# Kernel tuning notes

Measured on AMD Instinct MI355X. Metric: run time of the kernel, lower is better.

Reference implementation:

```python
import jax, jax.numpy as jnp
import numpy as np

N = 10000
E = 320000
D_IN = 512
D_OUT = 256


def setup_inputs() -> dict:
    key = jax.random.key(0)
    ks = jax.random.split(key, 10)
    x = jax.random.normal(ks[0], (N, D_IN), dtype=jnp.float32)
    edge_index = jax.random.randint(ks[1], (2, E), 0, N, dtype=jnp.int64)
    s_in = 1.0 / np.sqrt(D_IN)
    s_out = 1.0 / np.sqrt(D_OUT)
    W0 = jax.random.uniform(ks[2], (D_IN, D_OUT), minval=-s_in, maxval=s_in, dtype=jnp.float32)
    b0 = jax.random.uniform(ks[3], (D_OUT,), minval=-s_in, maxval=s_in, dtype=jnp.float32)
    Wl1 = jax.random.uniform(ks[4], (D_OUT, D_OUT), minval=-s_out, maxval=s_out, dtype=jnp.float32)
    bl1 = jax.random.uniform(ks[5], (D_OUT,), minval=-s_out, maxval=s_out, dtype=jnp.float32)
    Wr1 = jax.random.uniform(ks[6], (D_OUT, D_OUT), minval=-s_out, maxval=s_out, dtype=jnp.float32)
    Wl2 = jax.random.uniform(ks[7], (D_OUT, D_OUT), minval=-s_out, maxval=s_out, dtype=jnp.float32)
    bl2 = jax.random.uniform(ks[8], (D_OUT,), minval=-s_out, maxval=s_out, dtype=jnp.float32)
    Wr2 = jax.random.uniform(ks[9], (D_OUT, D_OUT), minval=-s_out, maxval=s_out, dtype=jnp.float32)
    return {"x": x, "edge_index": edge_index, "W0": W0, "b0": b0,
            "Wl1": Wl1, "bl1": bl1, "Wr1": Wr1,
            "Wl2": Wl2, "bl2": bl2, "Wr2": Wr2}


def _sage_conv(h, src, dst, Wl, bl, Wr):
    # mean aggregation over incoming edges: msg j->i uses h[src], summed at dst
    msg = h[src]                                        # [E, D]
    agg = jax.ops.segment_sum(msg, dst, num_segments=N)  # [N, D]
    deg = jax.ops.segment_sum(jnp.ones((msg.shape[0],), h.dtype), dst, num_segments=N)
    mean = agg / jnp.maximum(deg, 1.0)[:, None]
    return mean @ Wl + bl + h @ Wr


def reference(x, edge_index, W0, b0, Wl1, bl1, Wr1, Wl2, bl2, Wr2):
    src, dst = edge_index[0], edge_index[1]
    h = x @ W0 + b0                 # lin; dropout = identity (eval mode)
    out1 = jax.nn.relu(_sage_conv(h, src, dst, Wl1, bl1, Wr1)) + h
    out2 = _sage_conv(out1, src, dst, Wl2, bl2, Wr2) + out1
    return (out1, out2)
```

## Files before the change

kernel.cpp:

```cpp
#include <hip/hip_runtime.h>
#include <cstdint>

#define N_NODES 10000
#define N_EDGES 320000
#define DIN 512
#define DOUT 256
#define DEG_CAP 96

using short8 = __attribute__((ext_vector_type(8))) short;
using f32x4  = __attribute__((ext_vector_type(4))) float;
typedef unsigned short ushort_t;

static __device__ __forceinline__ unsigned short f2bf(float f) {
  unsigned u = __builtin_bit_cast(unsigned, f);
  u += 0x7fffu + ((u >> 16) & 1u);
  return (unsigned short)(u >> 16);
}
static __device__ __forceinline__ float bf2f(unsigned short s) {
  unsigned u = ((unsigned)s) << 16;
  return __builtin_bit_cast(float, u);
}

static __device__ __forceinline__ int detect64(const unsigned* ei) {
  unsigned z = 0;
  #pragma unroll
  for (int i = 1; i < 32; i += 2) z |= ei[i];
  return z == 0u;
}
static __device__ __forceinline__ int load_idx(const unsigned* ei, int i, int is64) {
  return is64 ? (int)ei[2 * i] : (int)ei[i];
}

#define B_EDGE 1250
#define B_W    1536
#define B_X    5000
__global__ __launch_bounds__(256) void prep_all(
    const unsigned* __restrict__ ei, int* __restrict__ cnt,
    int* __restrict__ srcs,
    const float* __restrict__ x, ushort_t* __restrict__ xb,
    const float* __restrict__ W0,
    const float* __restrict__ Wl1, const float* __restrict__ Wr1,
    const float* __restrict__ Wl2, const float* __restrict__ Wr2,
    ushort_t* __restrict__ W0T, ushort_t* __restrict__ WT1,
    ushort_t* __restrict__ WT2) {
  int b = blockIdx.x;
  if (b < B_EDGE) {
    int is64 = detect64(ei);
    int e = b * 256 + threadIdx.x;
    int d = load_idx(ei, N_EDGES + e, is64);
    int s = load_idx(ei, e, is64);
    int pos = atomicAdd(&cnt[d], 1);
    if (pos < DEG_CAP) srcs[d * DEG_CAP + pos] = s;
  } else if (b < B_EDGE + B_W) {
    int g = (b - B_EDGE) * 256 + threadIdx.x;
    int mat = g >> 17;
    int r = g & 131071;
    int n = r >> 9, k = r & 511;
    float v;
    ushort_t* dst;
    if (mat == 0)      { v = W0[k * 256 + n]; dst = W0T; }
    else if (mat == 1) { v = (k < 256) ? Wl1[k * 256 + n] : Wr1[(k - 256) * 256 + n]; dst = WT1; }
    else               { v = (k < 256) ? Wl2[k * 256 + n] : Wr2[(k - 256) * 256 + n]; dst = WT2; }
    dst[r] = f2bf(v);
  } else {
    int g = (b - B_EDGE - B_W) * 256 + threadIdx.x;
    float4 f = *(const float4*)(x + (size_t)g * 4);
    uint2 o;
    o.x = (unsigned)f2bf(f.x) | ((unsigned)f2bf(f.y) << 16);
    o.y = (unsigned)f2bf(f.z) | ((unsigned)f2bf(f.w) << 16);
    *(uint2*)(xb + (size_t)g * 4) = o;
  }
}

__global__ __launch_bounds__(256) void agg_mean(const ushort_t* __restrict__ h,
                                                const int* __restrict__ cnt,
                                                const int* __restrict__ srcs,
                                                ushort_t* __restrict__ mean) {
  int node = blockIdx.x * 4 + (threadIdx.x >> 6);
  int lane = threadIdx.x & 63;
  if (node >= N_NODES) return;
  int deg = cnt[node];
  int d = (deg < DEG_CAP) ? deg : DEG_CAP;
  int beg = node * DEG_CAP;
  int end = beg + d;
  float a0 = 0.f, a1 = 0.f, a2 = 0.f, a3 = 0.f;
  int j = beg;
  for (; j + 16 <= end; j += 16) {
    int4 sa = *(const int4*)(srcs + j);
    int4 sb = *(const int4*)(srcs + j + 4);
    int4 sc = *(const int4*)(srcs + j + 8);
    int4 sd = *(const int4*)(srcs + j + 12);
    uint2 u0 = *(const uint2*)(h + (size_t)sa.x * 256 + lane * 4);
    uint2 u1 = *(const uint2*)(h + (size_t)sa.y * 256 + lane * 4);
    uint2 u2 = *(const uint2*)(h + (size_t)sa.z * 256 + lane * 4);
    uint2 u3 = *(const uint2*)(h + (size_t)sa.w * 256 + lane * 4);
    uint2 u4 = *(const uint2*)(h + (size_t)sb.x * 256 + lane * 4);
    uint2 u5 = *(const uint2*)(h + (size_t)sb.y * 256 + lane * 4);
    uint2 u6 = *(const uint2*)(h + (size_t)sb.z * 256 + lane * 4);
    uint2 u7 = *(const uint2*)(h + (size_t)sb.w * 256 + lane * 4);
    uint2 u8 = *(const uint2*)(h + (size_t)sc.x * 256 + lane * 4);
    uint2 u9 = *(const uint2*)(h + (size_t)sc.y * 256 + lane * 4);
    uint2 ua = *(const uint2*)(h + (size_t)sc.z * 256 + lane * 4);
    uint2 ub = *(const uint2*)(h + (size_t)sc.w * 256 + lane * 4);
    uint2 uc = *(const uint2*)(h + (size_t)sd.x * 256 + lane * 4);
    uint2 ud = *(const uint2*)(h + (size_t)sd.y * 256 + lane * 4);
    uint2 ue = *(const uint2*)(h + (size_t)sd.z * 256 + lane * 4);
    uint2 uf = *(const uint2*)(h + (size_t)sd.w * 256 + lane * 4);
    a0 += bf2f(u0.x & 0xffff) + bf2f(u1.x & 0xffff) + bf2f(u2.x & 0xffff) + bf2f(u3.x & 0xffff);
    a1 += bf2f(u0.x >> 16)    + bf2f(u1.x >> 16)    + bf2f(u2.x >> 16)    + bf2f(u3.x >> 16);
    a2 += bf2f(u0.y & 0xffff) + bf2f(u1.y & 0xffff) + bf2f(u2.y & 0xffff) + bf2f(u3.y & 0xffff);
    a3 += bf2f(u0.y >> 16)    + bf2f(u1.y >> 16)    + bf2f(u2.y >> 16)    + bf2f(u3.y >> 16);
    a0 += bf2f(u4.x & 0xffff) + bf2f(u5.x & 0xffff) + bf2f(u6.x & 0xffff) + bf2f(u7.x & 0xffff);
    a1 += bf2f(u4.x >> 16)    + bf2f(u5.x >> 16)    + bf2f(u6.x >> 16)    + bf2f(u7.x >> 16);
    a2 += bf2f(u4.y & 0xffff) + bf2f(u5.y & 0xffff) + bf2f(u6.y & 0xffff) + bf2f(u7.y & 0xffff);
    a3 += bf2f(u4.y >> 16)    + bf2f(u5.y >> 16)    + bf2f(u6.y >> 16)    + bf2f(u7.y >> 16);
    a0 += bf2f(u8.x & 0xffff) + bf2f(u9.x & 0xffff) + bf2f(ua.x & 0xffff) + bf2f(ub.x & 0xffff);
    a1 += bf2f(u8.x >> 16)    + bf2f(u9.x >> 16)    + bf2f(ua.x >> 16)    + bf2f(ub.x >> 16);
    a2 += bf2f(u8.y & 0xffff) + bf2f(u9.y & 0xffff) + bf2f(ua.y & 0xffff) + bf2f(ub.y & 0xffff);
    a3 += bf2f(u8.y >> 16)    + bf2f(u9.y >> 16)    + bf2f(ua.y >> 16)    + bf2f(ub.y >> 16);
    a0 += bf2f(uc.x & 0xffff) + bf2f(ud.x & 0xffff) + bf2f(ue.x & 0xffff) + bf2f(uf.x & 0xffff);
    a1 += bf2f(uc.x >> 16)    + bf2f(ud.x >> 16)    + bf2f(ue.x >> 16)    + bf2f(uf.x >> 16);
    a2 += bf2f(uc.y & 0xffff) + bf2f(ud.y & 0xffff) + bf2f(ue.y & 0xffff) + bf2f(uf.y & 0xffff);
    a3 += bf2f(uc.y >> 16)    + bf2f(ud.y >> 16)    + bf2f(ue.y >> 16)    + bf2f(uf.y >> 16);
  }
  for (; j + 8 <= end; j += 8) {
    int4 sa = *(const int4*)(srcs + j);
    int4 sb = *(const int4*)(srcs + j + 4);
    uint2 u0 = *(const uint2*)(h + (size_t)sa.x * 256 + lane * 4);
    uint2 u1 = *(const uint2*)(h + (size_t)sa.y * 256 + lane * 4);
    uint2 u2 = *(const uint2*)(h + (size_t)sa.z * 256 + lane * 4);
    uint2 u3 = *(const uint2*)(h + (size_t)sa.w * 256 + lane * 4);
    uint2 u4 = *(const uint2*)(h + (size_t)sb.x * 256 + lane * 4);
    uint2 u5 = *(const uint2*)(h + (size_t)sb.y * 256 + lane * 4);
    uint2 u6 = *(const uint2*)(h + (size_t)sb.z * 256 + lane * 4);
    uint2 u7 = *(const uint2*)(h + (size_t)sb.w * 256 + lane * 4);
    a0 += bf2f(u0.x & 0xffff) + bf2f(u1.x & 0xffff) + bf2f(u2.x & 0xffff) + bf2f(u3.x & 0xffff);
    a1 += bf2f(u0.x >> 16)    + bf2f(u1.x >> 16)    + bf2f(u2.x >> 16)    + bf2f(u3.x >> 16);
    a2 += bf2f(u0.y & 0xffff) + bf2f(u1.y & 0xffff) + bf2f(u2.y & 0xffff) + bf2f(u3.y & 0xffff);
    a3 += bf2f(u0.y >> 16)    + bf2f(u1.y >> 16)    + bf2f(u2.y >> 16)    + bf2f(u3.y >> 16);
    a0 += bf2f(u4.x & 0xffff) + bf2f(u5.x & 0xffff) + bf2f(u6.x & 0xffff) + bf2f(u7.x & 0xffff);
    a1 += bf2f(u4.x >> 16)    + bf2f(u5.x >> 16)    + bf2f(u6.x >> 16)    + bf2f(u7.x >> 16);
    a2 += bf2f(u4.y & 0xffff) + bf2f(u5.y & 0xffff) + bf2f(u6.y & 0xffff) + bf2f(u7.y & 0xffff);
    a3 += bf2f(u4.y >> 16)    + bf2f(u5.y >> 16)    + bf2f(u6.y >> 16)    + bf2f(u7.y >> 16);
  }
  for (; j + 4 <= end; j += 4) {
    int4 s4 = *(const int4*)(srcs + j);
    uint2 u0 = *(const uint2*)(h + (size_t)s4.x * 256 + lane * 4);
    uint2 u1 = *(const uint2*)(h + (size_t)s4.y * 256 + lane * 4);
    uint2 u2 = *(const uint2*)(h + (size_t)s4.z * 256 + lane * 4);
    uint2 u3 = *(const uint2*)(h + (size_t)s4.w * 256 + lane * 4);
    a0 += bf2f(u0.x & 0xffff) + bf2f(u1.x & 0xffff) + bf2f(u2.x & 0xffff) + bf2f(u3.x & 0xffff);
    a1 += bf2f(u0.x >> 16)    + bf2f(u1.x >> 16)    + bf2f(u2.x >> 16)    + bf2f(u3.x >> 16);
    a2 += bf2f(u0.y & 0xffff) + bf2f(u1.y & 0xffff) + bf2f(u2.y & 0xffff) + bf2f(u3.y & 0xffff);
    a3 += bf2f(u0.y >> 16)    + bf2f(u1.y >> 16)    + bf2f(u2.y >> 16)    + bf2f(u3.y >> 16);
  }
  for (; j < end; ++j) {
    int s0 = srcs[j];
    uint2 u0 = *(const uint2*)(h + (size_t)s0 * 256 + lane * 4);
    a0 += bf2f(u0.x & 0xffff);
    a1 += bf2f(u0.x >> 16);
    a2 += bf2f(u0.y & 0xffff);
    a3 += bf2f(u0.y >> 16);
  }
  float inv = 1.0f / (float)(d > 1 ? d : 1);
  a0 *= inv; a1 *= inv; a2 *= inv; a3 *= inv;
  uint2 o;
  o.x = (unsigned)f2bf(a0) | ((unsigned)f2bf(a1) << 16);
  o.y = (unsigned)f2bf(a2) | ((unsigned)f2bf(a3) << 16);
  *(uint2*)(mean + (size_t)node * 256 + lane * 4) = o;
}

template<int DO_RELU, int HAS_ADD, int HAS_OUTF, int HAS_OUTB, int SPLIT_A>
__global__ __launch_bounds__(256) void gemm_pan(
    const ushort_t* __restrict__ A0, const ushort_t* __restrict__ A1,
    const ushort_t* __restrict__ BT, const float* __restrict__ bias,
    const ushort_t* __restrict__ addB,
    float* __restrict__ outF, ushort_t* __restrict__ outB, int M) {
  __shared__ ushort_t Bs[64 * 520];

  const int bid = blockIdx.x;
  const int sg  = bid >> 5;
  const int r32 = bid & 31;
  const int xt  = (sg << 3) + (r32 & 7);
  const int yt  = r32 >> 3;
  const int xtiles = (M + 127) >> 7;
  if (xt >= xtiles) return;

  const int tid  = threadIdx.x;
  const int lane = tid & 63;
  const int w    = tid >> 6;
  const int bn   = yt * 64;
  const int mbase = xt * 128 + w * 32;

  #pragma unroll
  for (int i = 0; i < 16; ++i) {
    int c = i * 256 + tid;
    int row = c >> 6;
    int c8  = (c & 63) * 8;
    uint4 bv = *(const uint4*)(BT + (size_t)(bn + row) * 512 + c8);
    *(uint4*)&Bs[row * 520 + c8] = bv;
  }
  __syncthreads();

  f32x4 acc[2][4] = {};
  const int mrow = lane & 15;
  const int k8   = (lane >> 4) * 8;

  #pragma unroll
  for (int kt = 0; kt < 512; kt += 32) {
    const ushort_t* Asrc;
    int acol, ald;
    if (SPLIT_A) {
      if (kt < 256) { Asrc = A0; acol = kt; } else { Asrc = A1; acol = kt - 256; }
      ald = 256;
    } else {
      Asrc = A0; acol = kt; ald = 512;
    }
    short8 a[2], b[4];
    #pragma unroll
    for (int s = 0; s < 2; ++s) {
      int row = mbase + s * 16 + mrow;
      a[s] = *(const short8*)(Asrc + (size_t)row * ald + acol + k8);
    }
    #pragma unroll
    for (int ni = 0; ni < 4; ++ni)
      b[ni] = *(const short8*)&Bs[(ni * 16 + mrow) * 520 + kt + k8];
    #pragma unroll
    for (int s = 0; s < 2; ++s)
      #pragma unroll
      for (int ni = 0; ni < 4; ++ni)
        acc[s][ni] = __builtin_amdgcn_mfma_f32_16x16x32_bf16(a[s], b[ni], acc[s][ni], 0, 0, 0);
  }

  const int cq   = lane >> 4;
  const int ccol = lane & 15;
  #pragma unroll
  for (int ni = 0; ni < 4; ++ni) {
    int gcol = bn + ni * 16 + ccol;
    float bv = bias[gcol];
    #pragma unroll
    for (int s = 0; s < 2; ++s) {
      #pragma unroll
      for (int r = 0; r < 4; ++r) {
        int grow = mbase + s * 16 + cq * 4 + r;
        if (grow < M) {
          float v = acc[s][ni][r] + bv;
          if (DO_RELU) v = fmaxf(v, 0.f);
          if (HAS_ADD) v += bf2f(addB[(size_t)grow * DOUT + gcol]);
          if (HAS_OUTF) __builtin_nontemporal_store(v, &outF[(size_t)grow * DOUT + gcol]);
          if (HAS_OUTB) outB[(size_t)grow * DOUT + gcol] = f2bf(v);
        }
      }
    }
  }
}

extern "C" void kernel_launch(void* const* d_in, const int* in_sizes, int n_in,
                              void* d_out, int out_size, void* d_ws, size_t ws_size,
                              hipStream_t stream) {
  const float*    x   = (const float*)d_in[0];
  const unsigned* ei  = (const unsigned*)d_in[1];
  const float*    W0  = (const float*)d_in[2];
  const float*    b0  = (const float*)d_in[3];
  const float*    Wl1 = (const float*)d_in[4];
  const float*    bl1 = (const float*)d_in[5];
  const float*    Wr1 = (const float*)d_in[6];
  const float*    Wl2 = (const float*)d_in[7];
  const float*    bl2 = (const float*)d_in[8];
  const float*    Wr2 = (const float*)d_in[9];

  char* ws = (char*)d_ws;
  size_t off = 0;
  auto alloc = [&](size_t bytes) {
    char* p = ws + off;
    off += (bytes + 255) & ~(size_t)255;
    return p;
  };
  ushort_t* xb  = (ushort_t*)alloc((size_t)N_NODES * 512 * 2);
  ushort_t* hb  = (ushort_t*)alloc((size_t)N_NODES * 256 * 2);
  ushort_t* o1b = (ushort_t*)alloc((size_t)N_NODES * 256 * 2);
  ushort_t* mb  = (ushort_t*)alloc((size_t)N_NODES * 256 * 2);
  ushort_t* W0T = (ushort_t*)alloc(256 * 512 * 2);
  ushort_t* WT1 = (ushort_t*)alloc(256 * 512 * 2);
  ushort_t* WT2 = (ushort_t*)alloc(256 * 512 * 2);
  int* cnt    = (int*)alloc(N_NODES * 4);
  int* srcs   = (int*)alloc((size_t)N_NODES * DEG_CAP * 4);

  float* out1 = (float*)d_out;
  float* out2 = out1 + (size_t)N_NODES * DOUT;

  hipMemsetAsync(cnt, 0, N_NODES * 4, stream);
  prep_all<<<B_EDGE + B_W + B_X, 256, 0, stream>>>(ei, cnt, srcs, x, xb,
                                                   W0, Wl1, Wr1, Wl2, Wr2,
                                                   W0T, WT1, WT2);

  const int GG = 320;
  gemm_pan<0, 0, 0, 1, 0><<<GG, 256, 0, stream>>>(xb, nullptr, W0T, b0, nullptr,
                                                  nullptr, hb, N_NODES);
  agg_mean<<<(N_NODES + 3) / 4, 256, 0, stream>>>(hb, cnt, srcs, mb);
  gemm_pan<1, 1, 1, 1, 1><<<GG, 256, 0, stream>>>(mb, hb, WT1, bl1, hb,
                                                  out1, o1b, N_NODES);
  agg_mean<<<(N_NODES + 3) / 4, 256, 0, stream>>>(o1b, cnt, srcs, mb);
  gemm_pan<0, 1, 1, 0, 1><<<GG, 256, 0, stream>>>(mb, o1b, WT2, bl2, o1b,
                                                  out2, nullptr, N_NODES);
}
```

Before: 196.0 us.

## Fuse root-weight GEMM into aggregation kernel and pre-pack weights in MFMA fragment layout

```diff
diff --git a/kernel.cpp b/kernel.cpp
--- a/kernel.cpp
+++ b/kernel.cpp
@@ -6,6 +6,7 @@
 #define DIN 512
 #define DOUT 256
 #define DEG_CAP 96
+#define AGGB 2500
 
 using short8 = __attribute__((ext_vector_type(8))) short;
 using f32x4  = __attribute__((ext_vector_type(4))) float;
@@ -41,8 +42,9 @@
     const float* __restrict__ W0,
     const float* __restrict__ Wl1, const float* __restrict__ Wr1,
     const float* __restrict__ Wl2, const float* __restrict__ Wr2,
-    ushort_t* __restrict__ W0T, ushort_t* __restrict__ WT1,
-    ushort_t* __restrict__ WT2) {
+    ushort_t* __restrict__ W0P,
+    ushort_t* __restrict__ WlP1, ushort_t* __restrict__ WrP1,
+    ushort_t* __restrict__ WlP2, ushort_t* __restrict__ WrP2) {
   int b = blockIdx.x;
   if (b < B_EDGE) {
     int is64 = detect64(ei);
@@ -55,13 +57,22 @@
     int g = (b - B_EDGE) * 256 + threadIdx.x;
     int mat = g >> 17;
     int r = g & 131071;
-    int n = r >> 9, k = r & 511;
-    float v;
-    ushort_t* dst;
-    if (mat == 0)      { v = W0[k * 256 + n]; dst = W0T; }
-    else if (mat == 1) { v = (k < 256) ? Wl1[k * 256 + n] : Wr1[(k - 256) * 256 + n]; dst = WT1; }
-    else               { v = (k < 256) ? Wl2[k * 256 + n] : Wr2[(k - 256) * 256 + n]; dst = WT2; }
-    dst[r] = f2bf(v);
+    if (mat == 0) {
+      int tile = r >> 9, e2 = r & 511;
+      int l = e2 >> 3, j = e2 & 7, q = l >> 4, rr = l & 15;
+      int nb = tile >> 4, kb = tile & 15;
+      int n = nb * 16 + rr, k = kb * 32 + q * 8 + j;
+      W0P[r] = f2bf(W0[k * 256 + n]);
+    } else {
+      int half = r >> 16, rr2 = r & 65535;
+      int tile = rr2 >> 9, e2 = rr2 & 511;
+      int l = e2 >> 3, j = e2 & 7, q = l >> 4, rr = l & 15;
+      int nb = tile >> 3, kb = tile & 7;
+      int n = nb * 16 + rr, k = kb * 32 + q * 8 + j;
+      const float* W = (mat == 1) ? (half ? Wr1 : Wl1) : (half ? Wr2 : Wl2);
+      ushort_t* P    = (mat == 1) ? (half ? WrP1 : WlP1) : (half ? WrP2 : WlP2);
+      P[rr2] = f2bf(W[k * 256 + n]);
+    }
   } else {
     int g = (b - B_EDGE - B_W) * 256 + threadIdx.x;
     float4 f = *(const float4*)(x + (size_t)g * 4);
@@ -72,13 +83,11 @@
   }
 }
 
-__global__ __launch_bounds__(256) void agg_mean(const ushort_t* __restrict__ h,
-                                                const int* __restrict__ cnt,
-                                                const int* __restrict__ srcs,
-                                                ushort_t* __restrict__ mean) {
-  int node = blockIdx.x * 4 + (threadIdx.x >> 6);
+static __device__ __forceinline__ void agg_body(
+    int grp, const ushort_t* __restrict__ h, const int* __restrict__ cnt,
+    const int* __restrict__ srcs, ushort_t* __restrict__ mean) {
+  int node = grp * 4 + (threadIdx.x >> 6);
   int lane = threadIdx.x & 63;
-  if (node >= N_NODES) return;
   int deg = cnt[node];
   int d = (deg < DEG_CAP) ? deg : DEG_CAP;
   int beg = node * DEG_CAP;
@@ -123,26 +132,6 @@
     a2 += bf2f(uc.y & 0xffff) + bf2f(ud.y & 0xffff) + bf2f(ue.y & 0xffff) + bf2f(uf.y & 0xffff);
     a3 += bf2f(uc.y >> 16)    + bf2f(ud.y >> 16)    + bf2f(ue.y >> 16)    + bf2f(uf.y >> 16);
   }
-  for (; j + 8 <= end; j += 8) {
-    int4 sa = *(const int4*)(srcs + j);
-    int4 sb = *(const int4*)(srcs + j + 4);
-    uint2 u0 = *(const uint2*)(h + (size_t)sa.x * 256 + lane * 4);
-    uint2 u1 = *(const uint2*)(h + (size_t)sa.y * 256 + lane * 4);
-    uint2 u2 = *(const uint2*)(h + (size_t)sa.z * 256 + lane * 4);
-    uint2 u3 = *(const uint2*)(h + (size_t)sa.w * 256 + lane * 4);
-    uint2 u4 = *(const uint2*)(h + (size_t)sb.x * 256 + lane * 4);
-    uint2 u5 = *(const uint2*)(h + (size_t)sb.y * 256 + lane * 4);
-    uint2 u6 = *(const uint2*)(h + (size_t)sb.z * 256 + lane * 4);
-    uint2 u7 = *(const uint2*)(h + (size_t)sb.w * 256 + lane * 4);
-    a0 += bf2f(u0.x & 0xffff) + bf2f(u1.x & 0xffff) + bf2f(u2.x & 0xffff) + bf2f(u3.x & 0xffff);
-    a1 += bf2f(u0.x >> 16)    + bf2f(u1.x >> 16)    + bf2f(u2.x >> 16)    + bf2f(u3.x >> 16);
-    a2 += bf2f(u0.y & 0xffff) + bf2f(u1.y & 0xffff) + bf2f(u2.y & 0xffff) + bf2f(u3.y & 0xffff);
-    a3 += bf2f(u0.y >> 16)    + bf2f(u1.y >> 16)    + bf2f(u2.y >> 16)    + bf2f(u3.y >> 16);
-    a0 += bf2f(u4.x & 0xffff) + bf2f(u5.x & 0xffff) + bf2f(u6.x & 0xffff) + bf2f(u7.x & 0xffff);
-    a1 += bf2f(u4.x >> 16)    + bf2f(u5.x >> 16)    + bf2f(u6.x >> 16)    + bf2f(u7.x >> 16);
-    a2 += bf2f(u4.y & 0xffff) + bf2f(u5.y & 0xffff) + bf2f(u6.y & 0xffff) + bf2f(u7.y & 0xffff);
-    a3 += bf2f(u4.y >> 16)    + bf2f(u5.y >> 16)    + bf2f(u6.y >> 16)    + bf2f(u7.y >> 16);
-  }
   for (; j + 4 <= end; j += 4) {
     int4 s4 = *(const int4*)(srcs + j);
     uint2 u0 = *(const uint2*)(h + (size_t)s4.x * 256 + lane * 4);
@@ -170,61 +159,39 @@
   *(uint2*)(mean + (size_t)node * 256 + lane * 4) = o;
 }
 
-template<int DO_RELU, int HAS_ADD, int HAS_OUTF, int HAS_OUTB, int SPLIT_A>
-__global__ __launch_bounds__(256) void gemm_pan(
-    const ushort_t* __restrict__ A0, const ushort_t* __restrict__ A1,
-    const ushort_t* __restrict__ BT, const float* __restrict__ bias,
-    const ushort_t* __restrict__ addB,
+template<int K, int BIAS, int ADDT, int RELU, int RES, int OUTF, int NTF, int OUTB, int ROT>
+static __device__ __forceinline__ void gemm_body(
+    int gbid, const ushort_t* __restrict__ A, const ushort_t* __restrict__ BP,
+    const float* __restrict__ bias, const float* __restrict__ tf,
+    const ushort_t* __restrict__ resB,
     float* __restrict__ outF, ushort_t* __restrict__ outB, int M) {
-  __shared__ ushort_t Bs[64 * 520];
-
-  const int bid = blockIdx.x;
-  const int sg  = bid >> 5;
-  const int r32 = bid & 31;
-  const int xt  = (sg << 3) + (r32 & 7);
+  constexpr int KT = K / 32;
+  const int sg  = gbid >> 5;
+  const int r32 = gbid & 31;
+  const int xt  = (sg << 3) + ((r32 + ROT) & 7);
   const int yt  = r32 >> 3;
-  const int xtiles = (M + 127) >> 7;
-  if (xt >= xtiles) return;
-
-  const int tid  = threadIdx.x;
-  const int lane = tid & 63;
-  const int w    = tid >> 6;
+  if (xt >= ((M + 127) >> 7)) return;
+  const int lane = threadIdx.x & 63;
+  const int w    = threadIdx.x >> 6;
   const int bn   = yt * 64;
   const int mbase = xt * 128 + w * 32;
-
-  #pragma unroll
-  for (int i = 0; i < 16; ++i) {
-    int c = i * 256 + tid;
-    int row = c >> 6;
-    int c8  = (c & 63) * 8;
-    uint4 bv = *(const uint4*)(BT + (size_t)(bn + row) * 512 + c8);
-    *(uint4*)&Bs[row * 520 + c8] = bv;
-  }
-  __syncthreads();
+  const int nb   = bn >> 4;
 
   f32x4 acc[2][4] = {};
   const int mrow = lane & 15;
   const int k8   = (lane >> 4) * 8;
 
   #pragma unroll
-  for (int kt = 0; kt < 512; kt += 32) {
-    const ushort_t* Asrc;
-    int acol, ald;
-    if (SPLIT_A) {
-      if (kt < 256) { Asrc = A0; acol = kt; } else { Asrc = A1; acol = kt - 256; }
-      ald = 256;
-    } else {
-      Asrc = A0; acol = kt; ald = 512;
-    }
+  for (int kt = 0; kt < K; kt += 32) {
     short8 a[2], b[4];
     #pragma unroll
     for (int s = 0; s < 2; ++s) {
       int row = mbase + s * 16 + mrow;
-      a[s] = *(const short8*)(Asrc + (size_t)row * ald + acol + k8);
+      a[s] = *(const short8*)(A + (size_t)row * K + kt + k8);
     }
     #pragma unroll
     for (int ni = 0; ni < 4; ++ni)
-      b[ni] = *(const short8*)&Bs[(ni * 16 + mrow) * 520 + kt + k8];
+      b[ni] = *(const short8*)(BP + ((size_t)(nb + ni) * KT + (kt >> 5)) * 512 + lane * 8);
     #pragma unroll
     for (int s = 0; s < 2; ++s)
       #pragma unroll
@@ -237,22 +204,58 @@
   #pragma unroll
   for (int ni = 0; ni < 4; ++ni) {
     int gcol = bn + ni * 16 + ccol;
-    float bv = bias[gcol];
+    float bv = BIAS ? bias[gcol] : 0.f;
     #pragma unroll
     for (int s = 0; s < 2; ++s) {
       #pragma unroll
       for (int r = 0; r < 4; ++r) {
         int grow = mbase + s * 16 + cq * 4 + r;
         if (grow < M) {
-          float v = acc[s][ni][r] + bv;
-          if (DO_RELU) v = fmaxf(v, 0.f);
-          if (HAS_ADD) v += bf2f(addB[(size_t)grow * DOUT + gcol]);
-          if (HAS_OUTF) __builtin_nontemporal_store(v, &outF[(size_t)grow * DOUT + gcol]);
-          if (HAS_OUTB) outB[(size_t)grow * DOUT + gcol] = f2bf(v);
+          size_t idx = (size_t)grow * DOUT + gcol;
+          float v = acc[s][ni][r];
+          if (BIAS) v += bv;
+          if (ADDT) v += tf[idx];
+          if (RELU) v = fmaxf(v, 0.f);
+          if (RES)  v += bf2f(resB[idx]);
+          if (OUTF) {
+            if (NTF) __builtin_nontemporal_store(v, &outF[idx]);
+            else     outF[idx] = v;
+          }
+          if (OUTB) outB[idx] = f2bf(v);
         }
       }
     }
   }
+}
+
+__global__ __launch_bounds__(256) void gemm1_k(
+    const ushort_t* __restrict__ xb, const ushort_t* __restrict__ W0P,
+    const float* __restrict__ b0, ushort_t* __restrict__ hb) {
+  gemm_body<512, 1, 0, 0, 0, 0, 0, 1, 0>(blockIdx.x, xb, W0P, b0, nullptr,
+                                         nullptr, nullptr, hb, N_NODES);
+}
+
+__global__ __launch_bounds__(256) void fused_agg_r(
+    const ushort_t* __restrict__ h, const int* __restrict__ cnt,
+    const int* __restrict__ srcs, ushort_t* __restrict__ mean,
+    const ushort_t* __restrict__ WrP, const float* __restrict__ bl,
+    float* __restrict__ tf) {
+  if (blockIdx.x < AGGB) {
+    agg_body(blockIdx.x, h, cnt, srcs, mean);
+  } else {
+    gemm_body<256, 1, 0, 0, 0, 1, 0, 0, 4>(blockIdx.x - AGGB, h, WrP, bl,
+                                           nullptr, nullptr, tf, nullptr,
+                                           N_NODES);
+  }
+}
+
+template<int RELU, int OUTB>
+__global__ __launch_bounds__(256) void gemmL_k(
+    const ushort_t* __restrict__ mb, const ushort_t* __restrict__ WlP,
+    const float* __restrict__ tf, const ushort_t* __restrict__ resB,
+    float* __restrict__ outF, ushort_t* __restrict__ outB) {
+  gemm_body<256, 0, 1, RELU, 1, 1, 1, OUTB, 0>(blockIdx.x, mb, WlP, nullptr,
+                                               tf, resB, outF, outB, N_NODES);
 }
 
 extern "C" void kernel_launch(void* const* d_in, const int* in_sizes, int n_in,
@@ -276,15 +279,18 @@
     off += (bytes + 255) & ~(size_t)255;
     return p;
   };
-  ushort_t* xb  = (ushort_t*)alloc((size_t)N_NODES * 512 * 2);
-  ushort_t* hb  = (ushort_t*)alloc((size_t)N_NODES * 256 * 2);
-  ushort_t* o1b = (ushort_t*)alloc((size_t)N_NODES * 256 * 2);
-  ushort_t* mb  = (ushort_t*)alloc((size_t)N_NODES * 256 * 2);
-  ushort_t* W0T = (ushort_t*)alloc(256 * 512 * 2);
-  ushort_t* WT1 = (ushort_t*)alloc(256 * 512 * 2);
-  ushort_t* WT2 = (ushort_t*)alloc(256 * 512 * 2);
-  int* cnt    = (int*)alloc(N_NODES * 4);
-  int* srcs   = (int*)alloc((size_t)N_NODES * DEG_CAP * 4);
+  ushort_t* xb   = (ushort_t*)alloc((size_t)N_NODES * 512 * 2);
+  ushort_t* hb   = (ushort_t*)alloc((size_t)N_NODES * 256 * 2);
+  ushort_t* o1b  = (ushort_t*)alloc((size_t)N_NODES * 256 * 2);
+  ushort_t* mb   = (ushort_t*)alloc((size_t)N_NODES * 256 * 2);
+  float*    tf   = (float*)   alloc((size_t)N_NODES * 256 * 4);
+  ushort_t* W0P  = (ushort_t*)alloc(256 * 512 * 2);
+  ushort_t* WlP1 = (ushort_t*)alloc(256 * 256 * 2);
+  ushort_t* WrP1 = (ushort_t*)alloc(256 * 256 * 2);
+  ushort_t* WlP2 = (ushort_t*)alloc(256 * 256 * 2);
+  ushort_t* WrP2 = (ushort_t*)alloc(256 * 256 * 2);
+  int* cnt  = (int*)alloc(N_NODES * 4);
+  int* srcs = (int*)alloc((size_t)N_NODES * DEG_CAP * 4);
 
   float* out1 = (float*)d_out;
   float* out2 = out1 + (size_t)N_NODES * DOUT;
@@ -292,15 +298,12 @@
   hipMemsetAsync(cnt, 0, N_NODES * 4, stream);
   prep_all<<<B_EDGE + B_W + B_X, 256, 0, stream>>>(ei, cnt, srcs, x, xb,
                                                    W0, Wl1, Wr1, Wl2, Wr2,
-                                                   W0T, WT1, WT2);
+                                                   W0P, WlP1, WrP1, WlP2, WrP2);
 
   const int GG = 320;
-  gemm_pan<0, 0, 0, 1, 0><<<GG, 256, 0, stream>>>(xb, nullptr, W0T, b0, nullptr,
-                                                  nullptr, hb, N_NODES);
-  agg_mean<<<(N_NODES + 3) / 4, 256, 0, stream>>>(hb, cnt, srcs, mb);
-  gemm_pan<1, 1, 1, 1, 1><<<GG, 256, 0, stream>>>(mb, hb, WT1, bl1, hb,
-                                                  out1, o1b, N_NODES);
-  agg_mean<<<(N_NODES + 3) / 4, 256, 0, stream>>>(o1b, cnt, srcs, mb);
-  gemm_pan<0, 1, 1, 0, 1><<<GG, 256, 0, stream>>>(mb, o1b, WT2, bl2, o1b,
-                                                  out2, nullptr, N_NODES);
-}
+  gemm1_k<<<GG, 256, 0, stream>>>(xb, W0P, b0, hb);
+  fused_agg_r<<<AGGB + GG, 256, 0, stream>>>(hb, cnt, srcs, mb, WrP1, bl1, tf);
+  gemmL_k<1, 1><<<GG, 256, 0, stream>>>(mb, WlP1, tf, hb, out1, o1b);
+  fused_agg_r<<<AGGB + GG, 256, 0, stream>>>(o1b, cnt, srcs, mb, WrP2, bl2, tf);
+  gemmL_k<0, 0><<<GG, 256, 0, stream>>>(mb, WlP2, tf, o1b, out2, nullptr);
+}
```

After: 219.9 us. 1.12x slower.
